# Kernel optimization log

Hardware: AMD Instinct MI355X
Metric: run time of the kernel (lower is better)

## Reference

```python
import jax, jax.numpy as jnp
import numpy as np

B, S, D, H, HD, L, W, MLP = 1, 4096, 1024, 16, 64, 3, 512, 4096
NB = S // W
EPS = 1e-5

def _layer_norm(x, g, b):
    m = jnp.mean(x, axis=-1, keepdims=True)
    v = jnp.mean(jnp.square(x - m), axis=-1, keepdims=True)
    return (x - m) * jax.lax.rsqrt(v + EPS) * g + b

def _rotate_half(x):
    x1, x2 = jnp.split(x, 2, axis=-1)
    return jnp.concatenate([-x2, x1], axis=-1)

def setup_inputs() -> dict:
    key = jax.random.key(0)
    ks = jax.random.split(key, 12)
    def nrm(k, shape):
        return jax.random.normal(k, shape, jnp.float32) * 0.02
    return {
        'hidden_states': jax.random.normal(ks[0], (B, S, D), jnp.float32),
        'position_ids': jnp.broadcast_to(jnp.arange(S, dtype=jnp.int32), (B, S)),
        'ln1_g': jnp.ones((L, D), jnp.float32), 'ln1_b': jnp.zeros((L, D), jnp.float32),
        'wq': nrm(ks[1], (L, D, D)), 'bq': jnp.zeros((L, D), jnp.float32),
        'wk': nrm(ks[2], (L, D, D)), 'bk': jnp.zeros((L, D), jnp.float32),
        'wv': nrm(ks[3], (L, D, D)), 'bv': jnp.zeros((L, D), jnp.float32),
        'wo': nrm(ks[4], (L, D, D)), 'bo': jnp.zeros((L, D), jnp.float32),
        'ln2_g': jnp.ones((L, D), jnp.float32), 'ln2_b': jnp.zeros((L, D), jnp.float32),
        'w1': nrm(ks[5], (L, D, MLP)), 'b1': jnp.zeros((L, MLP), jnp.float32),
        'w2': nrm(ks[6], (L, MLP, D)), 'b2': jnp.zeros((L, D), jnp.float32),
        'fln_g': jnp.ones((D,), jnp.float32), 'fln_b': jnp.zeros((D,), jnp.float32),
    }

def reference(hidden_states, position_ids, ln1_g, ln1_b, wq, bq, wk, bk, wv, bv,
              wo, bo, ln2_g, ln2_b, w1, b1, w2, b2, fln_g, fln_b):
    # RoPE tables (half-split / LLaMA convention)
    inv_freq = 1.0 / (10000.0 ** (jnp.arange(0, HD, 2, dtype=jnp.float32) / HD))
    ang = position_ids.astype(jnp.float32)[..., None] * inv_freq          # [B,S,HD/2]
    cos = jnp.concatenate([jnp.cos(ang)] * 2, axis=-1)[:, :, None, :]     # [B,S,1,HD]
    sin = jnp.concatenate([jnp.sin(ang)] * 2, axis=-1)[:, :, None, :]

    # causal sliding-window mask over (query-in-block, key-in-2-blocks)
    qi = jnp.arange(W)[:, None]
    kj = jnp.arange(2 * W)[None, :]
    rel = qi + W - kj                                                     # = i - j globally
    base = (rel >= 0) & (rel < W)                                         # [W,2W]
    valid = jnp.ones((NB, 2 * W), bool).at[0, :W].set(False)              # no keys before t=0
    mask = base[None, :, :] & valid[:, None, :]                           # [NB,W,2W]
    scale = HD ** -0.5

    x = hidden_states
    for l in range(L):
        h = _layer_norm(x, ln1_g[l], ln1_b[l])
        q = (h @ wq[l] + bq[l]).reshape(B, S, H, HD)
        k = (h @ wk[l] + bk[l]).reshape(B, S, H, HD)
        v = (h @ wv[l] + bv[l]).reshape(B, S, H, HD)
        q = q * cos + _rotate_half(q) * sin
        k = k * cos + _rotate_half(k) * sin
        qb = q.reshape(B, NB, W, H, HD)
        # keys/values for block b = [block b-1, block b] (pad one block in front)
        kp = jnp.pad(k, ((0, 0), (W, 0), (0, 0), (0, 0)))
        vp = jnp.pad(v, ((0, 0), (W, 0), (0, 0), (0, 0)))
        k2 = jnp.concatenate([kp[:, :-W].reshape(B, NB, W, H, HD),
                              kp[:, W:].reshape(B, NB, W, H, HD)], axis=2)  # [B,NB,2W,H,HD]
        v2 = jnp.concatenate([vp[:, :-W].reshape(B, NB, W, H, HD),
                              vp[:, W:].reshape(B, NB, W, H, HD)], axis=2)
        s = jnp.einsum('bnqhd,bnkhd->bnhqk', qb, k2) * scale              # [B,NB,H,W,2W]
        s = jnp.where(mask[None, :, None, :, :], s, -1e30)
        a = jax.nn.softmax(s, axis=-1)
        o = jnp.einsum('bnhqk,bnkhd->bnqhd', a, v2).reshape(B, S, D)
        x = x + (o @ wo[l] + bo[l])
        h = _layer_norm(x, ln2_g[l], ln2_b[l])
        m = jax.nn.gelu(h @ w1[l] + b1[l], approximate=False) @ w2[l] + b2[l]
        x = x + m
    return _layer_norm(x, fln_g, fln_b)
```

## Files before the change

kernel.cpp:

```cpp
#include <hip/hip_runtime.h>

typedef unsigned short u16;
typedef short s8v __attribute__((ext_vector_type(8)));
typedef float f4v __attribute__((ext_vector_type(4)));

__device__ __forceinline__ float bf2f(u16 u){ return __uint_as_float(((unsigned)u)<<16); }
__device__ __forceinline__ u16 f2bf(float f){
  unsigned u = __float_as_uint(f);
  unsigned r = u + 0x7fffu + ((u>>16)&1u);
  return (u16)(r>>16);
}
__device__ __forceinline__ void gload16(const void* g, void* l){
  __builtin_amdgcn_global_load_lds((const __attribute__((address_space(1))) void*)g,
                                   (__attribute__((address_space(3))) void*)l, 16, 0, 0);
}

struct TJobs {
  const float* src[18];
  u16* dst[18];
  int R[18];
  int C[18];
  int start[19];
};

__global__ __launch_bounds__(256) void transpose_pack(TJobs jb){
  __shared__ float tile[32][33];
  int bid = blockIdx.x;
  int j = 0;
  while (bid >= jb.start[j+1]) j++;
  int t = bid - jb.start[j];
  int C = jb.C[j], R = jb.R[j];
  int ctiles = C >> 5;
  int ty = t / ctiles, tx = t - ty*ctiles;
  const float* src = jb.src[j];
  u16* dst = jb.dst[j];
  int tid = threadIdx.x;
  #pragma unroll
  for (int i=0;i<4;i++){
    int e = tid*4 + i;
    int lr = e >> 5, lc = e & 31;
    tile[lr][lc] = src[(long)(ty*32+lr)*C + tx*32+lc];
  }
  __syncthreads();
  #pragma unroll
  for (int i=0;i<4;i++){
    int e = tid*4 + i;
    int lc = e >> 5, lr = e & 31;
    dst[(long)(tx*32+lc)*R + ty*32+lr] = f2bf(tile[lr][lc]);
  }
}

__global__ __launch_bounds__(256) void pack_bias(const float* __restrict__ bq, const float* __restrict__ bk,
                                                 const float* __restrict__ bv, float* __restrict__ outp){
  int t = blockIdx.x*256 + threadIdx.x;
  if (t >= 3*3072) return;
  int l = t / 3072, c = t - l*3072;
  float v = (c < 1024) ? bq[l*1024+c] : (c < 2048) ? bk[l*1024+c-1024] : bv[l*1024+c-2048];
  outp[t] = v;
}

__global__ __launch_bounds__(256) void rope_table(const int* __restrict__ pos, float* __restrict__ cosT,
                                                  float* __restrict__ sinT){
  int t = blockIdx.x*256 + threadIdx.x;
  int j = t & 31, s = t >> 5;
  float f = expf(-(float)j * 0.28782313662425572f);
  float ang = (float)pos[s] * f;
  cosT[t] = cosf(ang);
  sinT[t] = sinf(ang);
}

__global__ __launch_bounds__(256) void rope_apply(const u16* __restrict__ qkv, const float* __restrict__ cosT,
                                                  const float* __restrict__ sinT, u16* __restrict__ qr,
                                                  u16* __restrict__ kr, u16* __restrict__ vr){
  int t = blockIdx.x*256 + threadIdx.x;
  int j = t & 31, h = (t>>5) & 15, s = t >> 9;
  float c = cosT[(s<<5)+j], sn = sinT[(s<<5)+j];
  long base = (long)s*3072 + h*64 + j;
  long ob   = (long)s*1024 + h*64 + j;
  float q0 = bf2f(qkv[base]),      q1 = bf2f(qkv[base+32]);
  float k0 = bf2f(qkv[base+1024]), k1 = bf2f(qkv[base+1056]);
  qr[ob] = f2bf(q0*c - q1*sn);  qr[ob+32] = f2bf(q1*c + q0*sn);
  kr[ob] = f2bf(k0*c - k1*sn);  kr[ob+32] = f2bf(k1*c + k0*sn);
  vr[ob] = qkv[base+2048];      vr[ob+32] = qkv[base+2080];
}

__device__ __forceinline__ float block_sum(float v, float* red, int tid){
  #pragma unroll
  for (int m=1;m<64;m<<=1) v += __shfl_xor(v, m);
  int w = tid >> 6;
  if ((tid & 63) == 0) red[w] = v;
  __syncthreads();
  float r = red[0]+red[1]+red[2]+red[3];
  __syncthreads();
  return r;
}

template<int OUTF32>
__global__ __launch_bounds__(256) void ln_kernel(const float* __restrict__ x, const float* __restrict__ g,
                                                 const float* __restrict__ b, float* __restrict__ outF,
                                                 u16* __restrict__ outH){
  __shared__ float red[4];
  long row = blockIdx.x;
  int tid = threadIdx.x;
  const float4 xv = *reinterpret_cast<const float4*>(x + row*1024 + tid*4);
  float s = xv.x + xv.y + xv.z + xv.w;
  float mean = block_sum(s, red, tid) * (1.0f/1024.0f);
  float d0 = xv.x-mean, d1 = xv.y-mean, d2 = xv.z-mean, d3 = xv.w-mean;
  float ss = d0*d0 + d1*d1 + d2*d2 + d3*d3;
  float var = block_sum(ss, red, tid) * (1.0f/1024.0f);
  float rstd = rsqrtf(var + 1e-5f);
  int c = tid*4;
  const float4 gv = *reinterpret_cast<const float4*>(g + c);
  const float4 bv = *reinterpret_cast<const float4*>(b + c);
  float y0 = d0*rstd*gv.x + bv.x, y1 = d1*rstd*gv.y + bv.y;
  float y2 = d2*rstd*gv.z + bv.z, y3 = d3*rstd*gv.w + bv.w;
  if (OUTF32){
    float4 o; o.x=y0; o.y=y1; o.z=y2; o.w=y3;
    *reinterpret_cast<float4*>(outF + row*1024 + c) = o;
  } else {
    outH[row*1024 + c+0] = f2bf(y0);
    outH[row*1024 + c+1] = f2bf(y1);
    outH[row*1024 + c+2] = f2bf(y2);
    outH[row*1024 + c+3] = f2bf(y3);
  }
}

template<int EPI>
__global__ __launch_bounds__(256) void gemm_bt(const u16* __restrict__ A, const u16* __restrict__ BT,
                                               const float* __restrict__ bias, const float* __restrict__ resid,
                                               float* __restrict__ outF, u16* __restrict__ outH,
                                               int M, int N, int K){
  __shared__ u16 As[2][4096];
  __shared__ u16 Bs[2][4096];
  const int tid = threadIdx.x;
  const int gx = N >> 7;
  const int nwg = gridDim.x;
  const int cpx = nwg >> 3;
  const int sbid = (blockIdx.x & 7) * cpx + (blockIdx.x >> 3);
  const int bn = sbid % gx, bm = sbid / gx;

  const int w = tid >> 6, lane = tid & 63;
  const int wr = w >> 1, wc = w & 1;
  const int l15 = lane & 15, k8 = (lane >> 4) * 8;

  f4v acc[4][4];
  #pragma unroll
  for (int i=0;i<4;i++)
    #pragma unroll
    for (int j=0;j<4;j++)
      acc[i][j] = (f4v){0.f,0.f,0.f,0.f};

  const int fe = tid * 8;
  const int r0 = fe >> 5, c0 = fe & 31;
  const u16* ga0 = A  + ((long)(bm*128 + r0))*K + c0;
  const u16* gb0 = BT + ((long)(bn*128 + r0))*K + c0;
  const u16* ga1 = ga0 + (long)64*K;
  const u16* gb1 = gb0 + (long)64*K;

  const int nt = K >> 5;
  gload16(ga0, &As[0][fe]);
  gload16(ga1, &As[0][fe + 2048]);
  gload16(gb0, &Bs[0][fe]);
  gload16(gb1, &Bs[0][fe + 2048]);
  __syncthreads();

  int cur = 0;
  for (int t = 0; t < nt; ++t){
    if (t + 1 < nt){
      const int kn = (t + 1) << 5;
      gload16(ga0 + kn, &As[cur^1][fe]);
      gload16(ga1 + kn, &As[cur^1][fe + 2048]);
      gload16(gb0 + kn, &Bs[cur^1][fe]);
      gload16(gb1 + kn, &Bs[cur^1][fe + 2048]);
    }
    s8v af[4], bfr[4];
    #pragma unroll
    for (int i=0;i<4;i++){
      af[i]  = *(const s8v*)&As[cur][(wr*64 + i*16 + l15)*32 + k8];
      bfr[i] = *(const s8v*)&Bs[cur][(wc*64 + i*16 + l15)*32 + k8];
    }
    #pragma unroll
    for (int mi=0;mi<4;mi++)
      #pragma unroll
      for (int nf=0;nf<4;nf++)
        acc[mi][nf] = __builtin_amdgcn_mfma_f32_16x16x32_bf16(af[mi], bfr[nf], acc[mi][nf], 0, 0, 0);
    __syncthreads();
    cur ^= 1;
  }

  const int r4 = (lane >> 4) * 4;
  #pragma unroll
  for (int mi=0;mi<4;mi++){
    int row = bm*128 + wr*64 + mi*16 + r4;
    #pragma unroll
    for (int nf=0;nf<4;nf++){
      int col = bn*128 + wc*64 + nf*16 + l15;
      float bcol = bias[col];
      #pragma unroll
      for (int r=0;r<4;r++){
        float v = acc[mi][nf][r] + bcol;
        long idx = (long)(row + r)*N + col;
        if (EPI == 0){
          outH[idx] = f2bf(v);
        } else if (EPI == 1){
          outF[idx] = resid[idx] + v;
        } else {
          float gl = 0.5f*v*(1.0f + erff(v*0.70710678118654752f));
          outH[idx] = f2bf(gl);
        }
      }
    }
  }
}

__global__ __launch_bounds__(256) void attn_kernel(const u16* __restrict__ qr, const u16* __restrict__ kr,
                                                   const u16* __restrict__ vr, u16* __restrict__ ao){
  __shared__ u16 Pl[4][1280];
  __shared__ u16 Vl[4][2304];
  const int tid = threadIdx.x, w = tid >> 6, lane = tid & 63;
  const int task = blockIdx.x*4 + w;
  const int head = task >> 7;
  const int q0 = (task & 127) * 32;
  const int l15 = lane & 15, lg = lane >> 4, k8 = lg * 8;

  s8v aq[2][2];
  #pragma unroll
  for (int mi=0;mi<2;mi++)
    #pragma unroll
    for (int kf=0;kf<2;kf++)
      aq[mi][kf] = *(const s8v*)&qr[(long)(q0 + mi*16 + l15)*1024 + head*64 + kf*32 + k8];

  f4v o[2][4];
  #pragma unroll
  for (int i=0;i<2;i++)
    #pragma unroll
    for (int j=0;j<4;j++)
      o[i][j] = (f4v){0.f,0.f,0.f,0.f};
  float mrun[2][4], lrun[2][4];
  #pragma unroll
  for (int i=0;i<2;i++)
    #pragma unroll
    for (int r=0;r<4;r++){ mrun[i][r] = -1e30f; lrun[i][r] = 0.f; }

  const int ktlo = (q0 >= 512) ? ((q0 - 511) >> 5) : 0;
  const int kthi = (q0 + 31) >> 5;

  for (int kt = ktlo; kt <= kthi; ++kt){
    const int k0 = kt * 32;
    #pragma unroll
    for (int t=0;t<4;t++){
      int e = t*64 + lane;
      int r = e >> 3, c8 = (e & 7) * 8;
      *(s8v*)&Vl[w][r*72 + c8] = *(const s8v*)&vr[(long)(k0 + r)*1024 + head*64 + c8];
    }
    s8v bk[2][2];
    #pragma unroll
    for (int nf=0;nf<2;nf++)
      #pragma unroll
      for (int kf=0;kf<2;kf++)
        bk[nf][kf] = *(const s8v*)&kr[(long)(k0 + nf*16 + l15)*1024 + head*64 + kf*32 + k8];
    f4v s[2][2];
    #pragma unroll
    for (int mi=0;mi<2;mi++)
      #pragma unroll
      for (int nf=0;nf<2;nf++){
        f4v z = (f4v){0.f,0.f,0.f,0.f};
        z = __builtin_amdgcn_mfma_f32_16x16x32_bf16(aq[mi][0], bk[nf][0], z, 0,0,0);
        z = __builtin_amdgcn_mfma_f32_16x16x32_bf16(aq[mi][1], bk[nf][1], z, 0,0,0);
        s[mi][nf] = z;
      }
    float alpha[2][4];
    #pragma unroll
    for (int mi=0;mi<2;mi++){
      #pragma unroll
      for (int r=0;r<4;r++){
        int q = q0 + mi*16 + lg*4 + r;
        int kk0 = k0 + l15, kk1 = k0 + 16 + l15;
        bool ok0 = (kk0 <= q) && (q - kk0 < 512);
        bool ok1 = (kk1 <= q) && (q - kk1 < 512);
        float sv0 = ok0 ? s[mi][0][r]*0.125f : -1e30f;
        float sv1 = ok1 ? s[mi][1][r]*0.125f : -1e30f;
        float tm = fmaxf(sv0, sv1);
        tm = fmaxf(tm, __shfl_xor(tm, 1));
        tm = fmaxf(tm, __shfl_xor(tm, 2));
        tm = fmaxf(tm, __shfl_xor(tm, 4));
        tm = fmaxf(tm, __shfl_xor(tm, 8));
        float mnew = fmaxf(mrun[mi][r], tm);
        float al = __expf(mrun[mi][r] - mnew);
        float p0 = ok0 ? __expf(sv0 - mnew) : 0.f;
        float p1 = ok1 ? __expf(sv1 - mnew) : 0.f;
        float rs = p0 + p1;
        rs += __shfl_xor(rs, 1);
        rs += __shfl_xor(rs, 2);
        rs += __shfl_xor(rs, 4);
        rs += __shfl_xor(rs, 8);
        mrun[mi][r] = mnew;
        lrun[mi][r] = lrun[mi][r]*al + rs;
        alpha[mi][r] = al;
        s[mi][0][r] = p0;
        s[mi][1][r] = p1;
      }
      #pragma unroll
      for (int df=0;df<4;df++)
        #pragma unroll
        for (int r=0;r<4;r++)
          o[mi][df][r] *= alpha[mi][r];
    }
    #pragma unroll
    for (int mi=0;mi<2;mi++)
      #pragma unroll
      for (int nf=0;nf<2;nf++)
        #pragma unroll
        for (int r=0;r<4;r++)
          Pl[w][(mi*16 + lg*4 + r)*40 + nf*16 + l15] = f2bf(s[mi][nf][r]);
    s8v ap[2];
    #pragma unroll
    for (int mi=0;mi<2;mi++)
      ap[mi] = *(const s8v*)&Pl[w][(mi*16 + l15)*40 + k8];
    s8v bv[4];
    #pragma unroll
    for (int df=0;df<4;df++){
      #pragma unroll
      for (int i=0;i<8;i++)
        bv[df][i] = (short)Vl[w][(k8 + i)*72 + df*16 + l15];
    }
    #pragma unroll
    for (int mi=0;mi<2;mi++)
      #pragma unroll
      for (int df=0;df<4;df++)
        o[mi][df] = __builtin_amdgcn_mfma_f32_16x16x32_bf16(ap[mi], bv[df], o[mi][df], 0,0,0);
  }
  #pragma unroll
  for (int mi=0;mi<2;mi++)
    #pragma unroll
    for (int df=0;df<4;df++)
      #pragma unroll
      for (int r=0;r<4;r++){
        long row = q0 + mi*16 + lg*4 + r;
        int col = head*64 + df*16 + l15;
        ao[row*1024 + col] = f2bf(o[mi][df][r] / lrun[mi][r]);
      }
}

extern "C" void kernel_launch(void* const* d_in, const int* in_sizes, int n_in,
                              void* d_out, int out_size, void* d_ws, size_t ws_size,
                              hipStream_t stream){
  const float* hidden = (const float*)d_in[0];
  const int*   pos    = (const int*)d_in[1];
  const float* ln1_g  = (const float*)d_in[2];
  const float* ln1_b  = (const float*)d_in[3];
  const float* wq     = (const float*)d_in[4];
  const float* bq     = (const float*)d_in[5];
  const float* wk     = (const float*)d_in[6];
  const float* bk     = (const float*)d_in[7];
  const float* wv     = (const float*)d_in[8];
  const float* bv     = (const float*)d_in[9];
  const float* wo     = (const float*)d_in[10];
  const float* bo     = (const float*)d_in[11];
  const float* ln2_g  = (const float*)d_in[12];
  const float* ln2_b  = (const float*)d_in[13];
  const float* w1     = (const float*)d_in[14];
  const float* b1     = (const float*)d_in[15];
  const float* w2     = (const float*)d_in[16];
  const float* b2     = (const float*)d_in[17];
  const float* fg     = (const float*)d_in[18];
  const float* fb     = (const float*)d_in[19];
  float* out = (float*)d_out;

  char* ws = (char*)d_ws;
  size_t off = 0;
  auto alloc = [&](size_t bytes)->char*{
    char* p = ws + off;
    off = (off + bytes + 255) & ~(size_t)255;
    return p;
  };
  u16*   WQKVT = (u16*)  alloc(3ull*3072*1024*2);
  u16*   WOT   = (u16*)  alloc(3ull*1024*1024*2);
  u16*   W1T   = (u16*)  alloc(3ull*4096*1024*2);
  u16*   W2T   = (u16*)  alloc(3ull*1024*4096*2);
  float* BQKV  = (float*)alloc(3ull*3072*4);
  float* COS   = (float*)alloc(4096ull*32*4);
  float* SIN   = (float*)alloc(4096ull*32*4);
  float* X     = (float*)alloc(4096ull*1024*4);
  u16*   HB    = (u16*)  alloc(4096ull*1024*2);
  u16*   QKV   = (u16*)  alloc(4096ull*3072*2);
  u16*   QR    = (u16*)  alloc(4096ull*1024*2);
  u16*   KR    = (u16*)  alloc(4096ull*1024*2);
  u16*   VR    = (u16*)  alloc(4096ull*1024*2);
  u16*   AO    = (u16*)  alloc(4096ull*1024*2);
  u16*   MB    = (u16*)  alloc(4096ull*4096*2);

  TJobs jb;
  int total = 0, ji = 0;
  for (int l=0;l<3;l++){
    const float* srcs[6] = { wq + (size_t)l*1024*1024, wk + (size_t)l*1024*1024, wv + (size_t)l*1024*1024,
                             wo + (size_t)l*1024*1024, w1 + (size_t)l*1024*4096, w2 + (size_t)l*4096*1024 };
    u16* dsts[6] = { WQKVT + (size_t)l*3072*1024, WQKVT + (size_t)l*3072*1024 + 1024*1024,
                     WQKVT + (size_t)l*3072*1024 + 2048*1024, WOT + (size_t)l*1024*1024,
                     W1T + (size_t)l*4096*1024, W2T + (size_t)l*1024*4096 };
    int Rs[6] = {1024,1024,1024,1024,1024,4096};
    int Cs[6] = {1024,1024,1024,1024,4096,1024};
    for (int k=0;k<6;k++){
      jb.src[ji] = srcs[k]; jb.dst[ji] = dsts[k]; jb.R[ji] = Rs[k]; jb.C[ji] = Cs[k];
      jb.start[ji] = total;
      total += (Rs[k]/32)*(Cs[k]/32);
      ji++;
    }
  }
  jb.start[18] = total;

  transpose_pack<<<total, 256, 0, stream>>>(jb);
  pack_bias<<<36, 256, 0, stream>>>(bq, bk, bv, BQKV);
  rope_table<<<512, 256, 0, stream>>>(pos, COS, SIN);

  for (int l=0;l<3;l++){
    const float* xin = (l == 0) ? hidden : X;
    ln_kernel<0><<<4096, 256, 0, stream>>>(xin, ln1_g + l*1024, ln1_b + l*1024, nullptr, HB);
    gemm_bt<0><<<24*32, 256, 0, stream>>>(HB, WQKVT + (size_t)l*3072*1024, BQKV + l*3072,
                                          nullptr, nullptr, QKV, 4096, 3072, 1024);
    rope_apply<<<8192, 256, 0, stream>>>(QKV, COS, SIN, QR, KR, VR);
    attn_kernel<<<512, 256, 0, stream>>>(QR, KR, VR, AO);
    gemm_bt<1><<<8*32, 256, 0, stream>>>(AO, WOT + (size_t)l*1024*1024, bo + l*1024,
                                         xin, X, nullptr, 4096, 1024, 1024);
    ln_kernel<0><<<4096, 256, 0, stream>>>(X, ln2_g + l*1024, ln2_b + l*1024, nullptr, HB);
    gemm_bt<2><<<32*32, 256, 0, stream>>>(HB, W1T + (size_t)l*4096*1024, b1 + l*4096,
                                          nullptr, nullptr, MB, 4096, 4096, 1024);
    gemm_bt<1><<<8*32, 256, 0, stream>>>(MB, W2T + (size_t)l*1024*4096, b2 + l*1024,
                                         X, X, nullptr, 4096, 1024, 4096);
  }
  ln_kernel<1><<<4096, 256, 0, stream>>>(X, fg, fb, out, nullptr);
}
```

Measured before the change: 1.021 ms.

## Add 256x256-tile GEMM kernel for QKV and MLP-up projections

Introduces a new 512-thread GEMM with 256x256 output tiles, 64-wide K steps, double-buffered direct global-to-LDS loads with XOR swizzle, and setprio around the MFMA bursts. It replaces the 128x128 gemm_bt for the QKV projection and the first MLP GEMM, with bias and exact GELU in the epilogue. The aim is higher arithmetic intensity and fewer LDS reloads per FLOP. In exchange the grids shrink to 192 and 256 workgroups, which may leave some of the 256 CUs idle for QKV and raises register and LDS pressure (128KB LDS per block).

```diff
diff --git a/kernel.cpp b/kernel.cpp
--- a/kernel.cpp
+++ b/kernel.cpp
@@ -126,6 +126,117 @@
 }
 
 template<int EPI>
+__global__ __launch_bounds__(512, 2) void gemm256(const u16* __restrict__ A, const u16* __restrict__ BT,
+                                                  const float* __restrict__ bias,
+                                                  u16* __restrict__ outH, int N, int K){
+  __shared__ u16 LA[2][16384];
+  __shared__ u16 LB[2][16384];
+  const int tid = threadIdx.x;
+  const int gx = N >> 8;
+  const int cpx = gridDim.x >> 3;
+  const int sbid = (blockIdx.x & 7) * cpx + (blockIdx.x >> 3);
+  const int bn = sbid % gx, bm = sbid / gx;
+  const int w = tid >> 6, lane = tid & 63;
+  const int wr = w >> 2, wc = w & 3;
+  const int l15 = lane & 15, lg = lane >> 4;
+
+  const int srow = tid >> 3;
+  const int c16s = (tid & 7) ^ (srow & 7);
+  const u16* gA0 = A  + (long)(bm*256 + srow)*K + c16s*8;
+  const u16* gB0 = BT + (long)(bn*256 + srow)*K + c16s*8;
+  const long j64K = (long)64*K;
+  const int ldst = tid*8;
+
+  f4v acc[8][4];
+  #pragma unroll
+  for (int i=0;i<8;i++)
+    #pragma unroll
+    for (int j=0;j<4;j++)
+      acc[i][j] = (f4v){0.f,0.f,0.f,0.f};
+
+  const int swz = (l15 & 7);
+  const int cA0 = ((0*4 + lg) ^ swz) * 8;
+  const int cA1 = ((1*4 + lg) ^ swz) * 8;
+
+  #define STAGE(buf, k0) do { \
+    _Pragma("unroll") \
+    for (int j=0;j<4;j++) gload16(gA0 + (long)j*j64K + (k0), &LA[buf][j*4096 + ldst]); \
+    _Pragma("unroll") \
+    for (int j=0;j<4;j++) gload16(gB0 + (long)j*j64K + (k0), &LB[buf][j*4096 + ldst]); \
+  } while(0)
+
+  const int nt = K >> 6;
+  STAGE(0, 0);
+  STAGE(1, 64);
+  asm volatile("s_waitcnt vmcnt(8)" ::: "memory");
+  __builtin_amdgcn_s_barrier();
+  __builtin_amdgcn_sched_barrier(0);
+
+  for (int t = 0; t < nt; ++t){
+    const int buf = t & 1;
+    s8v bfr[4][2];
+    #pragma unroll
+    for (int nf=0;nf<4;nf++){
+      const int rb = (wc*64 + nf*16 + l15)*64;
+      bfr[nf][0] = *(const s8v*)&LB[buf][rb + cA0];
+      bfr[nf][1] = *(const s8v*)&LB[buf][rb + cA1];
+    }
+    #pragma unroll
+    for (int half=0; half<2; ++half){
+      s8v af[4][2];
+      #pragma unroll
+      for (int mi=0;mi<4;mi++){
+        const int ra = (wr*128 + half*64 + mi*16 + l15)*64;
+        af[mi][0] = *(const s8v*)&LA[buf][ra + cA0];
+        af[mi][1] = *(const s8v*)&LA[buf][ra + cA1];
+      }
+      __builtin_amdgcn_s_setprio(1);
+      #pragma unroll
+      for (int mi=0;mi<4;mi++)
+        #pragma unroll
+        for (int nf=0;nf<4;nf++){
+          acc[half*4+mi][nf] = __builtin_amdgcn_mfma_f32_16x16x32_bf16(af[mi][0], bfr[nf][0], acc[half*4+mi][nf], 0,0,0);
+          acc[half*4+mi][nf] = __builtin_amdgcn_mfma_f32_16x16x32_bf16(af[mi][1], bfr[nf][1], acc[half*4+mi][nf], 0,0,0);
+        }
+      __builtin_amdgcn_s_setprio(0);
+    }
+    __builtin_amdgcn_sched_barrier(0);
+    __builtin_amdgcn_s_barrier();
+    __builtin_amdgcn_sched_barrier(0);
+    if (t + 2 < nt){
+      STAGE(buf, (t+2) << 6);
+      asm volatile("s_waitcnt vmcnt(8)" ::: "memory");
+    } else {
+      asm volatile("s_waitcnt vmcnt(0)" ::: "memory");
+    }
+    __builtin_amdgcn_s_barrier();
+    __builtin_amdgcn_sched_barrier(0);
+  }
+  #undef STAGE
+
+  #pragma unroll
+  for (int mi=0;mi<8;mi++){
+    int row = bm*256 + wr*128 + mi*16 + lg*4;
+    #pragma unroll
+    for (int nf=0;nf<4;nf++){
+      int col = bn*256 + wc*64 + nf*16 + l15;
+      float bcol = bias[col];
+      #pragma unroll
+      for (int r=0;r<4;r++){
+        float v = acc[mi][nf][r] + bcol;
+        long idx = (long)(row + r)*N + col;
+        if (EPI == 0){
+          outH[idx] = f2bf(v);
+        } else {
+          float gl = 0.5f*v*(1.0f + erff(v*0.70710678118654752f));
+          outH[idx] = f2bf(gl);
+        }
+      }
+    }
+  }
+}
+
+template<int EPI>
 __global__ __launch_bounds__(256) void gemm_bt(const u16* __restrict__ A, const u16* __restrict__ BT,
                                                const float* __restrict__ bias, const float* __restrict__ resid,
                                                float* __restrict__ outF, u16* __restrict__ outH,
@@ -416,15 +527,15 @@
   for (int l=0;l<3;l++){
     const float* xin = (l == 0) ? hidden : X;
     ln_kernel<0><<<4096, 256, 0, stream>>>(xin, ln1_g + l*1024, ln1_b + l*1024, nullptr, HB);
-    gemm_bt<0><<<24*32, 256, 0, stream>>>(HB, WQKVT + (size_t)l*3072*1024, BQKV + l*3072,
-                                          nullptr, nullptr, QKV, 4096, 3072, 1024);
+    gemm256<0><<<12*16, 512, 0, stream>>>(HB, WQKVT + (size_t)l*3072*1024, BQKV + l*3072,
+                                          QKV, 3072, 1024);
     rope_apply<<<8192, 256, 0, stream>>>(QKV, COS, SIN, QR, KR, VR);
     attn_kernel<<<512, 256, 0, stream>>>(QR, KR, VR, AO);
     gemm_bt<1><<<8*32, 256, 0, stream>>>(AO, WOT + (size_t)l*1024*1024, bo + l*1024,
                                          xin, X, nullptr, 4096, 1024, 1024);
     ln_kernel<0><<<4096, 256, 0, stream>>>(X, ln2_g + l*1024, ln2_b + l*1024, nullptr, HB);
-    gemm_bt<2><<<32*32, 256, 0, stream>>>(HB, W1T + (size_t)l*4096*1024, b1 + l*4096,
-                                          nullptr, nullptr, MB, 4096, 4096, 1024);
+    gemm256<2><<<16*16, 512, 0, stream>>>(HB, W1T + (size_t)l*4096*1024, b1 + l*4096,
+                                          MB, 4096, 1024);
     gemm_bt<1><<<8*32, 256, 0, stream>>>(MB, W2T + (size_t)l*1024*4096, b2 + l*1024,
                                          X, X, nullptr, 4096, 1024, 4096);
   }
```

Measured after the change: 1.023 ms. No clear change (+0.3%).
